# Kernel optimization log

Hardware: AMD Instinct MI355X
Metric: run time of the kernel (lower is better)

The kernel has to match this reference:

```python
import jax, jax.numpy as jnp
import numpy as np

P0 = 2   # tublet_size
P = 16   # patch_size
FC = 2   # flow channels (map_x, map_y)


def patchify(x, p0, p1, p2):
    # x: (B, C, T, H, W) -> (B, (T/p0)(H/p1)(W/p2), p0*p1*p2*C)
    B, C, T, H, W = x.shape
    x = x.reshape(B, C, T // p0, p0, H // p1, p1, W // p2, p2)
    x = x.transpose(0, 2, 4, 6, 3, 5, 7, 1)  # b t h w p0 p1 p2 c
    return x.reshape(B, (T // p0) * (H // p1) * (W // p2), p0 * p1 * p2 * C)


def unpatchify(x, p0, p1, p2, C, T, H, W):
    # x: (B, N, p0*p1*p2*C) -> (B, C, T, H, W)
    B = x.shape[0]
    x = x.reshape(B, T // p0, H // p1, W // p2, p0, p1, p2, C)
    x = x.transpose(0, 7, 1, 4, 2, 5, 3, 6)  # b c t p0 h p1 w p2
    return x.reshape(B, C, T, H, W)


def bilinear_warp(imgs, mx, my):
    # imgs: (B, C, T, H, W); mx, my: (B, T, H, W) absolute sample coords.
    # Equivalent of cv2.remap INTER_LINEAR with constant (zero) border.
    B, C, T, H, W = imgs.shape
    x0 = jnp.floor(mx)
    y0 = jnp.floor(my)
    wx = (mx - x0).reshape(B, 1, T, H * W)
    wy = (my - y0).reshape(B, 1, T, H * W)
    x0i = x0.astype(jnp.int32)
    y0i = y0.astype(jnp.int32)
    imgs_flat = imgs.reshape(B, C, T, H * W)

    def gather(yi, xi):
        yc = jnp.clip(yi, 0, H - 1)
        xc = jnp.clip(xi, 0, W - 1)
        idx = (yc * W + xc).reshape(B, 1, T, H * W)
        v = jnp.take_along_axis(imgs_flat, jnp.broadcast_to(idx, (B, C, T, H * W)), axis=-1)
        valid = ((yi >= 0) & (yi <= H - 1) & (xi >= 0) & (xi <= W - 1)).reshape(B, 1, T, H * W)
        return v * valid.astype(v.dtype)

    v00 = gather(y0i, x0i)
    v01 = gather(y0i, x0i + 1)
    v10 = gather(y0i + 1, x0i)
    v11 = gather(y0i + 1, x0i + 1)
    out = (v00 * (1 - wx) * (1 - wy) + v01 * wx * (1 - wy)
           + v10 * (1 - wx) * wy + v11 * wx * wy)
    return out.reshape(B, C, T, H, W)


def setup_inputs() -> dict:
    key = jax.random.key(0)
    k1, k2, k3 = jax.random.split(key, 3)
    B, C, T, H, W = 8, 3, 16, 224, 224
    N = (T // P0) * (H // P) * (W // P)         # 1568 tokens
    D = P0 * P * P * FC                         # 1024 per-token flow dim
    output = jax.random.normal(k1, (B, N, D), dtype=jnp.float32)
    raw_target = jax.random.normal(k2, (B, C, T, H, W), dtype=jnp.float32)
    mask = jax.random.randint(k3, (B, N), 0, 2) > 0
    return {"output": output, "raw_target": raw_target, "mask": mask}


def reference(output, raw_target, mask):
    B, C, T, H, W = raw_target.shape
    # tokens -> dense flow field (B, 2, T, H, W)
    flows = unpatchify(output, P0, P, P, FC, T, H, W)
    gx = jnp.arange(W, dtype=flows.dtype)               # (W,)
    gy = jnp.arange(H, dtype=flows.dtype)[:, None]      # (H, 1)
    mx = flows[:, 0] + gx                                # (B, T, H, W)
    my = flows[:, 1] + gy
    recons = bilinear_warp(raw_target, mx, my)           # (B, C, T, H, W)
    rec_p = patchify(recons, P0, P, P)                   # (B, N, p0*p1*p2*C)
    tgt_p = patchify(raw_target, P0, P, P)
    m = mask.astype(rec_p.dtype)[..., None]              # (B, N, 1)
    diff2 = (rec_p - tgt_p) ** 2 * m
    denom = jnp.maximum(m.sum(), 1.0) * rec_p.shape[-1]
    return diff2.sum() / denom
```

## Files before the change

kernel.cpp:

```cpp
#include <hip/hip_runtime.h>

#define Bd 8
#define Cd 3
#define Td 16
#define Hd 224
#define Wd 224
#define Nd 1568
#define Dd 1024
#define HWd (Hd*Wd)
#define MASK_N (Bd*Nd)
#define PATCH_ELEMS 1536.0

#define WINP 16
#define PLANE 256
#define BUF (6*PLANE)
#define GRID_MAIN 2048
#define STG_V4 384

struct TokGeo { int b, t2, ph, pw; };

__device__ __forceinline__ TokGeo geo(int tk) {
    TokGeo g;
    g.b = tk / Nd;
    int n = tk - g.b * Nd;
    g.t2 = n / 196;
    int rem = n - g.t2 * 196;
    g.ph = rem / 14;
    g.pw = rem - g.ph * 14;
    return g;
}

__device__ __forceinline__ int stg_goff(int j) {
    int p   = j >> 6;
    int rem = j & 63;
    int r   = rem >> 2;
    int c4  = (rem & 3) << 2;
    return (p >> 1) * (16 * HWd) + (p & 1) * HWd + r * Wd + c4;
}

__device__ __forceinline__ float compute_tok(const float* __restrict__ raw,
                                             const float* __restrict__ pl0,
                                             const TokGeo& g, int tid,
                                             float2 f0, float2 f1) {
    const int WX = g.pw << 4, WY = g.ph << 4;
    const int h = WY + (tid >> 4);
    const int w = WX + (tid & 15);
    float acc = 0.f;
    #pragma unroll
    for (int i0 = 0; i0 < 2; ++i0) {
        float2 f = i0 ? f1 : f0;
        float mx = f.x + (float)w;
        float my = f.y + (float)h;

        float x0 = floorf(mx), y0 = floorf(my);
        float wx = mx - x0,    wy = my - y0;
        int x0i = (int)x0, y0i = (int)y0;
        int x1i = x0i + 1, y1i = y0i + 1;

        bool vx0 = (x0i >= 0) && (x0i < Wd);
        bool vx1 = (x1i >= 0) && (x1i < Wd);
        bool vy0 = (y0i >= 0) && (y0i < Hd);
        bool vy1 = (y1i >= 0) && (y1i < Hd);

        int xc0 = min(max(x0i, 0), Wd - 1);
        int xc1 = min(max(x1i, 0), Wd - 1);
        int yc0 = min(max(y0i, 0), Hd - 1);
        int yc1 = min(max(y1i, 0), Hd - 1);

        float w00 = (1.f - wx) * (1.f - wy) * ((vx0 && vy0) ? 1.f : 0.f);
        float w01 = wx         * (1.f - wy) * ((vx1 && vy0) ? 1.f : 0.f);
        float w10 = (1.f - wx) * wy         * ((vx0 && vy1) ? 1.f : 0.f);
        float w11 = wx         * wy         * ((vx1 && vy1) ? 1.f : 0.f);

        const int lx0 = xc0 - WX, lx1 = xc1 - WX;
        const int ly0 = yc0 - WY, ly1 = yc1 - WY;
        const bool ok = (lx0 >= 0) & (lx1 < WINP) & (ly0 >= 0) & (ly1 < WINP);

        if (ok) {
            const int b00 = (ly0 << 4) + lx0;
            const int b01 = (ly0 << 4) + lx1;
            const int b10 = (ly1 << 4) + lx0;
            const int b11 = (ly1 << 4) + lx1;
            #pragma unroll
            for (int c = 0; c < Cd; ++c) {
                const float* pl = pl0 + ((c << 1) | i0) * PLANE;
                float rec = pl[b00] * w00 + pl[b01] * w01
                          + pl[b10] * w10 + pl[b11] * w11;
                float d = rec - pl[tid & 255];
                acc += d * d;
            }
        } else {
            const int i00 = yc0 * Wd + xc0;
            const int i01 = yc0 * Wd + xc1;
            const int i10 = yc1 * Wd + xc0;
            const int i11 = yc1 * Wd + xc1;
            const float* base = raw + (size_t)(g.b * 48 + (g.t2 << 1) + i0) * HWd;
            #pragma unroll
            for (int c = 0; c < Cd; ++c) {
                const float* img = base + c * (16 * HWd);
                float rec = img[i00] * w00 + img[i01] * w01
                          + img[i10] * w10 + img[i11] * w11;
                const float* pl = pl0 + ((c << 1) | i0) * PLANE;
                float d = rec - pl[tid & 255];
                acc += d * d;
            }
        }
    }
    return acc;
}

__global__ void compact_kernel(const int* __restrict__ mask,
                               int* __restrict__ list,
                               unsigned int* __restrict__ cnt) {
    const int tid = threadIdx.x;
    __shared__ unsigned wt[16];
    unsigned base = 0;
    for (int i0 = 0; i0 < MASK_N; i0 += 1024) {
        int i = i0 + tid;
        bool m = (i < MASK_N) && (mask[i] != 0);
        unsigned long long bal = __ballot(m);
        int lane = tid & 63, wid = tid >> 6;
        unsigned pre  = (unsigned)__popcll(bal & ((1ull << lane) - 1ull));
        unsigned wtot = (unsigned)__popcll(bal);
        if (lane == 0) wt[wid] = wtot;
        __syncthreads();
        unsigned wbase = base;
        for (int k = 0; k < wid; ++k) wbase += wt[k];
        if (m) list[wbase + pre] = i;
        unsigned tot = 0;
        #pragma unroll
        for (int k = 0; k < 16; ++k) tot += wt[k];
        base += tot;
        __syncthreads();
    }
    if (tid == 0) *cnt = base;
}

__global__ __launch_bounds__(256, 6)
void flow_mse_main(const float* __restrict__ outp,
                   const float* __restrict__ raw,
                   const int* __restrict__ list,
                   const unsigned int* __restrict__ cntp,
                   float* __restrict__ partial) {
    __shared__ float lds[2 * BUF];
    __shared__ float sdata[4];
    const int tid = threadIdx.x;
    const int cnt = (int)*cntp;

    const int q0 = stg_goff(tid);
    const bool k1 = tid < (STG_V4 - 256);
    const int q1 = stg_goff(k1 ? tid + 256 : 0);
    const int l0 = tid << 2;
    const int l1 = (tid << 2) + 1024;

    float4 s0, s1;
    float2 fc0, fc1, fn0, fn1;
    TokGeo gc, gn;
    float acc = 0.f;

    int idx = blockIdx.x;
    int cur = 0;

    if (idx < cnt) {
        int tk = list[idx];
        gc = geo(tk);
        const float* base = raw + (size_t)(gc.b * 48 + (gc.t2 << 1)) * HWd
                          + (gc.ph << 4) * Wd + (gc.pw << 4);
        s0 = *(const float4*)(base + q0);
        if (k1) s1 = *(const float4*)(base + q1);
        const float2* fp = (const float2*)(outp + ((size_t)tk << 10));
        fc0 = fp[tid]; fc1 = fp[256 + tid];
        *(float4*)(lds + l0) = s0;
        if (k1) *(float4*)(lds + l1) = s1;
    }

    while (idx < cnt) {
        int nidx = idx + GRID_MAIN;
        __syncthreads();
        bool have_next = nidx < cnt;
        if (have_next) {
            int ntk = list[nidx];
            gn = geo(ntk);
            const float* base = raw + (size_t)(gn.b * 48 + (gn.t2 << 1)) * HWd
                              + (gn.ph << 4) * Wd + (gn.pw << 4);
            s0 = *(const float4*)(base + q0);
            if (k1) s1 = *(const float4*)(base + q1);
            const float2* fp = (const float2*)(outp + ((size_t)ntk << 10));
            fn0 = fp[tid]; fn1 = fp[256 + tid];
        }
        acc += compute_tok(raw, lds + cur * BUF, gc, tid, fc0, fc1);
        if (have_next) {
            float* dst = lds + (cur ^ 1) * BUF;
            *(float4*)(dst + l0) = s0;
            if (k1) *(float4*)(dst + l1) = s1;
        }
        idx = nidx; cur ^= 1;
        gc = gn; fc0 = fn0; fc1 = fn1;
    }

    for (int off = 32; off > 0; off >>= 1) acc += __shfl_down(acc, off, 64);
    if ((tid & 63) == 0) sdata[tid >> 6] = acc;
    __syncthreads();
    if (tid == 0)
        partial[blockIdx.x] = sdata[0] + sdata[1] + sdata[2] + sdata[3];
}

__global__ void finalize_kernel(const float* __restrict__ partial,
                                const unsigned int* __restrict__ cntp,
                                float* __restrict__ out) {
    double s = 0.0;
    for (int i = threadIdx.x; i < GRID_MAIN; i += blockDim.x)
        s += (double)partial[i];
    for (int off = 32; off > 0; off >>= 1)
        s += __shfl_down(s, off, 64);
    __shared__ double sdat[4];
    int lane = threadIdx.x & 63, wid = threadIdx.x >> 6;
    if (lane == 0) sdat[wid] = s;
    __syncthreads();
    if (threadIdx.x == 0) {
        double st = sdat[0] + sdat[1] + sdat[2] + sdat[3];
        unsigned ct = *cntp;
        double denom = (double)(ct > 0u ? ct : 1u) * PATCH_ELEMS;
        out[0] = (float)(st / denom);
    }
}

extern "C" void kernel_launch(void* const* d_in, const int* in_sizes, int n_in,
                              void* d_out, int out_size, void* d_ws, size_t ws_size,
                              hipStream_t stream) {
    const float* outp = (const float*)d_in[0];
    const float* raw  = (const float*)d_in[1];
    const int*   mask = (const int*)d_in[2];
    float* out = (float*)d_out;

    unsigned int* cnt = (unsigned int*)d_ws;
    float* partial = (float*)((char*)d_ws + 16);
    int*   list    = (int*)((char*)d_ws + 16 + GRID_MAIN * 4);

    compact_kernel<<<1, 1024, 0, stream>>>(mask, list, cnt);
    flow_mse_main<<<GRID_MAIN, 256, 0, stream>>>(outp, raw, list, cnt, partial);
    finalize_kernel<<<1, 256, 0, stream>>>(partial, cnt, out);
}
```

Before: 171.2 us.

## Batch all bilinear taps before arithmetic, halve grid, relax launch bounds

Restructures the per-token compute so the samples from both time slices and all three channels, plus the targets, are loaded into registers first. Only then are the weighted sums and squared differences evaluated. This gives more memory-level parallelism for the LDS and global gather latencies. The grid is halved to 1024 blocks and the occupancy hint in launch bounds is removed, trading occupancy for more registers per thread.

Result: no change. 170.0 us (-0.7%).

```diff
diff --git a/kernel.cpp b/kernel.cpp
--- a/kernel.cpp
+++ b/kernel.cpp
@@ -14,7 +14,7 @@
 #define WINP 16
 #define PLANE 256
 #define BUF (6*PLANE)
-#define GRID_MAIN 2048
+#define GRID_MAIN 1024
 #define STG_V4 384
 
 struct TokGeo { int b, t2, ph, pw; };
@@ -45,7 +45,10 @@
     const int WX = g.pw << 4, WY = g.ph << 4;
     const int h = WY + (tid >> 4);
     const int w = WX + (tid & 15);
-    float acc = 0.f;
+
+    float v00[2][3], v01[2][3], v10[2][3], v11[2][3], tg[2][3];
+    float W00[2], W01[2], W10[2], W11[2];
+
     #pragma unroll
     for (int i0 = 0; i0 < 2; ++i0) {
         float2 f = i0 ? f1 : f0;
@@ -67,14 +70,18 @@
         int yc0 = min(max(y0i, 0), Hd - 1);
         int yc1 = min(max(y1i, 0), Hd - 1);
 
-        float w00 = (1.f - wx) * (1.f - wy) * ((vx0 && vy0) ? 1.f : 0.f);
-        float w01 = wx         * (1.f - wy) * ((vx1 && vy0) ? 1.f : 0.f);
-        float w10 = (1.f - wx) * wy         * ((vx0 && vy1) ? 1.f : 0.f);
-        float w11 = wx         * wy         * ((vx1 && vy1) ? 1.f : 0.f);
+        W00[i0] = (1.f - wx) * (1.f - wy) * ((vx0 && vy0) ? 1.f : 0.f);
+        W01[i0] = wx         * (1.f - wy) * ((vx1 && vy0) ? 1.f : 0.f);
+        W10[i0] = (1.f - wx) * wy         * ((vx0 && vy1) ? 1.f : 0.f);
+        W11[i0] = wx         * wy         * ((vx1 && vy1) ? 1.f : 0.f);
 
         const int lx0 = xc0 - WX, lx1 = xc1 - WX;
         const int ly0 = yc0 - WY, ly1 = yc1 - WY;
         const bool ok = (lx0 >= 0) & (lx1 < WINP) & (ly0 >= 0) & (ly1 < WINP);
+
+        #pragma unroll
+        for (int c = 0; c < Cd; ++c)
+            tg[i0][c] = pl0[(((c << 1) | i0) * PLANE) + tid];
 
         if (ok) {
             const int b00 = (ly0 << 4) + lx0;
@@ -84,10 +91,10 @@
             #pragma unroll
             for (int c = 0; c < Cd; ++c) {
                 const float* pl = pl0 + ((c << 1) | i0) * PLANE;
-                float rec = pl[b00] * w00 + pl[b01] * w01
-                          + pl[b10] * w10 + pl[b11] * w11;
-                float d = rec - pl[tid & 255];
-                acc += d * d;
+                v00[i0][c] = pl[b00];
+                v01[i0][c] = pl[b01];
+                v10[i0][c] = pl[b10];
+                v11[i0][c] = pl[b11];
             }
         } else {
             const int i00 = yc0 * Wd + xc0;
@@ -98,12 +105,23 @@
             #pragma unroll
             for (int c = 0; c < Cd; ++c) {
                 const float* img = base + c * (16 * HWd);
-                float rec = img[i00] * w00 + img[i01] * w01
-                          + img[i10] * w10 + img[i11] * w11;
-                const float* pl = pl0 + ((c << 1) | i0) * PLANE;
-                float d = rec - pl[tid & 255];
-                acc += d * d;
+                v00[i0][c] = img[i00];
+                v01[i0][c] = img[i01];
+                v10[i0][c] = img[i10];
+                v11[i0][c] = img[i11];
             }
+        }
+    }
+
+    float acc = 0.f;
+    #pragma unroll
+    for (int i0 = 0; i0 < 2; ++i0) {
+        #pragma unroll
+        for (int c = 0; c < Cd; ++c) {
+            float rec = v00[i0][c] * W00[i0] + v01[i0][c] * W01[i0]
+                      + v10[i0][c] * W10[i0] + v11[i0][c] * W11[i0];
+            float d = rec - tg[i0][c];
+            acc += d * d;
         }
     }
     return acc;
@@ -136,7 +154,7 @@
     if (tid == 0) *cnt = base;
 }
 
-__global__ __launch_bounds__(256, 6)
+__global__ __launch_bounds__(256)
 void flow_mse_main(const float* __restrict__ outp,
                    const float* __restrict__ raw,
                    const int* __restrict__ list,
```
